# Performance work log

Hardware: AMD Instinct MI355X
Metric: run time of the kernel (lower is better)

## Reference

```python
import jax, jax.numpy as jnp
import numpy as np


def setup_inputs() -> dict:
    key = jax.random.key(0)
    ks = jax.random.split(key, 6)
    B, Cin, H, W = 8, 512, 128, 128
    Ck, Cv, K = 256, 256, 64
    s = lambda fan: fan ** -0.5
    return {
        "x": jax.random.normal(ks[0], (B, Cin, H, W), jnp.float32),
        "context": jax.random.normal(ks[1], (B, Cv, K), jnp.float32),
        "Wq": jax.random.normal(ks[2], (Ck, Cin), jnp.float32) * s(Cin),
        "Wk": jax.random.normal(ks[3], (Ck, Cv), jnp.float32) * s(Cv),
        "Wv": jax.random.normal(ks[4], (Cv, Cv), jnp.float32) * s(Cv),
        "Wp": jax.random.normal(ks[5], (Cin, Cv), jnp.float32) * s(Cv),
    }


def reference(x, context, Wq, Wk, Wv, Wp):
    B, Cin, H, W = x.shape
    Ck = Wq.shape[0]
    scale = Ck ** -0.5
    xf = x.reshape(B, Cin, H * W)                      # [B, Cin, N]
    q = jnp.einsum("kc,bcn->bnk", Wq, xf)             # [B, N, Ck]
    k = jnp.einsum("kc,bcm->bkm", Wk, context)        # [B, Ck, K]
    v = jnp.einsum("vc,bcm->bmv", Wv, context)        # [B, K, Cv]
    sim = jnp.einsum("bnk,bkm->bnm", q, k) * scale    # [B, N, K]
    attn = jax.nn.softmax(sim, axis=-1)
    out = jnp.einsum("bnm,bmv->bnv", attn, v)         # [B, N, Cv]
    out = jnp.einsum("cv,bnv->bcn", Wp, out)          # [B, Cin, N]
    return out.reshape(B, Cin, H, W)
```

## Files before the change

### kernel.cpp

```cpp
#include <hip/hip_runtime.h>
#include <stdint.h>

#define B_    8
#define CIN   512
#define NPIX  16384
#define CK    256
#define KCTX  64
#define CV    256

typedef _Float16 f16;
typedef _Float16 f16x4 __attribute__((ext_vector_type(4)));
typedef _Float16 f16x8 __attribute__((ext_vector_type(8)));
typedef float    f32x4 __attribute__((ext_vector_type(4)));

#define LOG2E 1.44269504f

#define WQK_OFF 0
#define WPV_OFF 524288

#define WAITVM(N) asm volatile("s_waitcnt vmcnt(" #N ")" ::: "memory")
#define LGKM0     asm volatile("s_waitcnt lgkmcnt(0)" ::: "memory")
#define SCHEDB    __builtin_amdgcn_sched_barrier(0)
#define SBAR      __builtin_amdgcn_s_barrier()

__device__ __forceinline__ void gl_lds16(const void* g, void* l) {
    __builtin_amdgcn_global_load_lds(
        (const __attribute__((address_space(1))) uint32_t*)g,
        (__attribute__((address_space(3))) uint32_t*)l, 16, 0, 0);
}

__global__ __launch_bounds__(1024) void prep(const float* __restrict__ ctx,
                                             const float* __restrict__ Wk,
                                             const float* __restrict__ Wv,
                                             const float* __restrict__ Wq,
                                             const float* __restrict__ Wp,
                                             char* __restrict__ ws) {
    __shared__ char lds[65536];
    char* ctx_t = lds;
    char* kv_s  = lds + 32768;

    const int p = blockIdx.x;
    const int b = blockIdx.y;
    const int path = p >> 1, h = p & 1;
    const int t = threadIdx.x;
    const int w = t >> 6, l = t & 63, g = l >> 4, ln = l & 15;

    {
        const int m4 = (t & 15) * 4, c4 = (t >> 4) * 4;
        const float* cp = ctx + (size_t)b * (CV * KCTX) + (size_t)c4 * KCTX + m4;
        f32x4 xr[4];
        #pragma unroll
        for (int i = 0; i < 4; ++i) xr[i] = *(const f32x4*)(cp + (size_t)i * KCTX);
        #pragma unroll
        for (int j = 0; j < 4; ++j) {
            f16x4 v4; v4[0] = (f16)xr[0][j]; v4[1] = (f16)xr[1][j]; v4[2] = (f16)xr[2][j]; v4[3] = (f16)xr[3][j];
            int m = m4 + j;
            *(f16x4*)(ctx_t + m * 512 + 16 * (((c4 >> 3) & 31) ^ (m & 7)) + 2 * (c4 & 7)) = v4;
        }
    }
    __syncthreads();

    {
        const float* W = path ? Wv : Wk;
        const int rbase = 64 * (w >> 2);
        const int mm = 16 * (w & 3) + ln;
        f32x4 acc[4] = {};
        for (int ks = 0; ks < 8; ++ks) {
            f16x8 bf = *(const f16x8*)(ctx_t + mm * 512 + 16 * ((4 * ks + g) ^ (mm & 7)));
            #pragma unroll
            for (int mi = 0; mi < 4; ++mi) {
                int row = rbase + 16 * mi + ln;
                const float* wp0 = W + (size_t)row * CV + 32 * ks + 8 * g;
                f32x4 lo = *(const f32x4*)wp0, hi = *(const f32x4*)(wp0 + 4);
                f16x8 af;
                #pragma unroll
                for (int j = 0; j < 4; ++j) { af[j] = (f16)lo[j]; af[4 + j] = (f16)hi[j]; }
                acc[mi] = __builtin_amdgcn_mfma_f32_16x16x32_f16(af, bf, acc[mi], 0, 0, 0);
            }
        }
        #pragma unroll
        for (int mi = 0; mi < 4; ++mi)
            #pragma unroll
            for (int r = 0; r < 4; ++r) {
                int row = rbase + 16 * mi + 4 * g + r;
                *(f16*)(kv_s + mm * 512 + 16 * ((((row >> 3) & 31)) ^ (mm & 7)) + 2 * (row & 7)) = (f16)acc[mi][r];
            }
    }
    __syncthreads();

    if (path == 0) {
        f32x4 acc2[4] = {};
        const int cA = 256 * h + 16 * w + ln;
        const float* qcol = Wq + cA;
        for (int ks = 0; ks < 8; ++ks) {
            f16x8 af;
            #pragma unroll
            for (int j = 0; j < 8; ++j)
                af[j] = (f16)qcol[(size_t)(32 * ks + 8 * g + j) * CIN];
            #pragma unroll
            for (int ni = 0; ni < 4; ++ni) {
                int m2 = 16 * ni + ln;
                f16x8 bf = *(const f16x8*)(kv_s + m2 * 512 + 16 * ((4 * ks + g) ^ (m2 & 7)));
                acc2[ni] = __builtin_amdgcn_mfma_f32_16x16x32_f16(af, bf, acc2[ni], 0, 0, 0);
            }
        }
        char* dst = ws + WQK_OFF + b * 65536;
        #pragma unroll
        for (int ni = 0; ni < 4; ++ni)
            #pragma unroll
            for (int r = 0; r < 4; ++r) {
                int c = 256 * h + 16 * w + 4 * g + r;
                int s  = c >> 6, kk = (c >> 5) & 1, gk = (c >> 3) & 3, j = c & 7;
                int byte = ((((s * 4 + ni) * 2 + kk) * 4 + gk) * 16 + ln) * 16 + 2 * j;
                *(f16*)(dst + byte) = (f16)(acc2[ni][r] * 0.0625f);
            }
    } else {
        f32x4 acc2[4] = {};
        const int cA = 256 * h + 16 * w + ln;
        for (int ks = 0; ks < 8; ++ks) {
            const float* pp = Wp + (size_t)cA * CV + 32 * ks + 8 * g;
            f32x4 lo = *(const f32x4*)pp, hi = *(const f32x4*)(pp + 4);
            f16x8 af;
            #pragma unroll
            for (int j = 0; j < 4; ++j) { af[j] = (f16)lo[j]; af[4 + j] = (f16)hi[j]; }
            #pragma unroll
            for (int ni = 0; ni < 4; ++ni) {
                int m2 = 16 * ni + ln;
                f16x8 bf = *(const f16x8*)(kv_s + m2 * 512 + 16 * ((4 * ks + g) ^ (m2 & 7)));
                acc2[ni] = __builtin_amdgcn_mfma_f32_16x16x32_f16(af, bf, acc2[ni], 0, 0, 0);
            }
        }
        char* dst = ws + WPV_OFF + b * 65536;
        #pragma unroll
        for (int ni = 0; ni < 4; ++ni) {
            const int kkm = ni >> 1;
            const int gm  = ln >> 2;
            const int jm  = 4 * (ni & 1) + (ln & 3);
            #pragma unroll
            for (int r = 0; r < 4; ++r) {
                int c = 256 * h + 16 * w + 4 * g + r;
                int ct = c >> 4, lnc = c & 15;
                int byte = (((ct * 2 + kkm) * 4 + gm) * 16 + lnc) * 16 + 2 * jm;
                *(f16*)(dst + byte) = (f16)acc2[ni][r];
            }
        }
    }
}

__global__ __launch_bounds__(1024) void fused(const float* __restrict__ x,
                                              const char* __restrict__ ws,
                                              float* __restrict__ out) {
    extern __shared__ char lds[];
    char* tab_l = lds;
    char* x_s   = lds + 65536;

    const int b = blockIdx.y;
    const int n0 = blockIdx.x * 256;
    const int t = threadIdx.x;
    const int w = t >> 6, l = t & 63, g = l >> 4, ln = l & 15;
    const int nB = 16 * w + ln;
    const int fnB = (nB ^ (nB >> 3)) & 7;

    const char* wqk_g = ws + WQK_OFF + b * 65536;
    const char* wpv_g = ws + WPV_OFF + b * 65536;
    const float* xb = x + (size_t)b * CIN * NPIX + n0;

    const int cg = t >> 6;
    const int n4 = 4 * (t & 63);

    f32x4 xr[2][4];

#define STAGE_LOAD(S, SLOT)                                                    \
    {                                                                          \
        const float* xp = xb + (size_t)(64 * (S) + 4 * cg) * NPIX + n4;        \
        asm volatile("global_load_dwordx4 %0, %1, off"                        \
                     : "=&v"(xr[SLOT][0]) : "v"(xp));                          \
        asm volatile("global_load_dwordx4 %0, %1, off"                        \
                     : "=&v"(xr[SLOT][1]) : "v"(xp + NPIX));                   \
        asm volatile("global_load_dwordx4 %0, %1, off"                        \
                     : "=&v"(xr[SLOT][2]) : "v"(xp + 2 * (size_t)NPIX));       \
        asm volatile("global_load_dwordx4 %0, %1, off"                        \
                     : "=&v"(xr[SLOT][3]) : "v"(xp + 3 * (size_t)NPIX));       \
    }

#define STAGE_WRITE(BUF, SLOT)                                                 \
    {                                                                          \
        _Pragma("unroll")                                                      \
        for (int j = 0; j < 4; ++j) {                                          \
            f16x4 v4;                                                          \
            v4[0] = (f16)xr[SLOT][0][j]; v4[1] = (f16)xr[SLOT][1][j];          \
            v4[2] = (f16)xr[SLOT][2][j]; v4[3] = (f16)xr[SLOT][3][j];          \
            int nl = n4 + j;                                                   \
            int fn = (nl ^ (nl >> 3)) & 7;                                     \
            *(f16x4*)((BUF) + nl * 128 + 16 * ((cg >> 1) ^ fn) + 8 * (cg & 1)) = v4; \
        }                                                                      \
    }

    #pragma unroll
    for (int r = 0; r < 4; ++r) {
        int ch = t + 1024 * r;
        gl_lds16(wqk_g + ch * 16, tab_l + ch * 16);
    }
    SCHEDB;
    STAGE_LOAD(0, 0); SCHEDB;
    STAGE_LOAD(1, 1); SCHEDB;
    WAITVM(4);
    SCHEDB;
    STAGE_WRITE(x_s, 0);
    LGKM0; SCHEDB; SBAR; SCHEDB;

    f32x4 accs[4] = {};
    #pragma unroll
    for (int s = 0; s < 8; ++s) {
        const char* xc = x_s + (s & 1) * 32768;
        #pragma unroll
        for (int kk = 0; kk < 2; ++kk) {
            f16x8 bf = *(const f16x8*)(xc + nB * 128 + 16 * ((4 * kk + g) ^ fnB));
            #pragma unroll
            for (int mi = 0; mi < 4; ++mi) {
                f16x8 af = *(const f16x8*)(tab_l + ((((s * 4 + mi) * 2 + kk) * 4 + g) * 16 + ln) * 16);
                accs[mi] = __builtin_amdgcn_mfma_f32_16x16x32_f16(af, bf, accs[mi], 0, 0, 0);
            }
        }
        SCHEDB;
        if (s < 7) {
            if (s < 6) { STAGE_LOAD(s + 2, (s & 1)); SCHEDB; }
            if (s < 6) { WAITVM(4); } else { WAITVM(0); }
            SCHEDB;
            STAGE_WRITE(x_s + ((s + 1) & 1) * 32768, ((s + 1) & 1));
            LGKM0;
        } else {
            LGKM0;
        }
        SCHEDB; SBAR; SCHEDB;
    }

    #pragma unroll
    for (int r = 0; r < 4; ++r) {
        int ch = t + 1024 * r;
        gl_lds16(wpv_g + ch * 16, tab_l + ch * 16);
    }

    float mx = accs[0][0];
    #pragma unroll
    for (int mi = 0; mi < 4; ++mi)
        #pragma unroll
        for (int r = 0; r < 4; ++r) mx = fmaxf(mx, accs[mi][r]);
    mx = fmaxf(mx, __shfl_xor(mx, 16, 64));
    mx = fmaxf(mx, __shfl_xor(mx, 32, 64));
    float pv[4][4];
    float sum = 0.f;
    #pragma unroll
    for (int mi = 0; mi < 4; ++mi)
        #pragma unroll
        for (int r = 0; r < 4; ++r) {
            float pe = __builtin_amdgcn_exp2f((accs[mi][r] - mx) * LOG2E);
            pv[mi][r] = pe; sum += pe;
        }
    sum += __shfl_xor(sum, 16, 64);
    sum += __shfl_xor(sum, 32, 64);
    float inv = 1.f / sum;

    f16x8 afr[2];
    #pragma unroll
    for (int kk = 0; kk < 2; ++kk)
        #pragma unroll
        for (int j = 0; j < 8; ++j)
            afr[kk][j] = (f16)(pv[2 * kk + (j >> 2)][j & 3] * inv);

    WAITVM(0); SCHEDB; SBAR; SCHEDB;

    float* ob = out + (size_t)b * CIN * NPIX + n0 + 16 * w + 4 * g;
    #pragma unroll 4
    for (int ct = 0; ct < 32; ++ct) {
        int c = 16 * ct + ln;
        f32x4 acc = {};
        #pragma unroll
        for (int kk = 0; kk < 2; ++kk) {
            f16x8 bfp = *(const f16x8*)(tab_l + (((ct * 2 + kk) * 4 + g) * 16 + ln) * 16);
            acc = __builtin_amdgcn_mfma_f32_16x16x32_f16(afr[kk], bfp, acc, 0, 0, 0);
        }
        *(f32x4*)(ob + (size_t)c * NPIX) = acc;
    }
}

extern "C" void kernel_launch(void* const* d_in, const int* in_sizes, int n_in,
                              void* d_out, int out_size, void* d_ws, size_t ws_size,
                              hipStream_t stream) {
    (void)in_sizes; (void)n_in; (void)out_size; (void)ws_size;
    const float* x   = (const float*)d_in[0];
    const float* ctx = (const float*)d_in[1];
    const float* Wq  = (const float*)d_in[2];
    const float* Wk  = (const float*)d_in[3];
    const float* Wv  = (const float*)d_in[4];
    const float* Wp  = (const float*)d_in[5];
    float* out = (float*)d_out;
    char* ws = (char*)d_ws;

    prep<<<dim3(4, B_), 1024, 0, stream>>>(ctx, Wk, Wv, Wq, Wp, ws);
    fused<<<dim3(NPIX / 256, B_), 1024, 131072, stream>>>(x, ws, out);
}
```

Baseline: 161.6 us.

## Double pixel tile per block and reuse weight fragments across two n-tiles

```diff
diff --git a/kernel.cpp b/kernel.cpp
--- a/kernel.cpp
+++ b/kernel.cpp
@@ -15,8 +15,8 @@
 
 #define LOG2E 1.44269504f
 
-#define WQK_OFF 0
-#define WPV_OFF 524288
+#define WQK_OFF  0
+#define WPV_OFF  524288
 
 #define WAITVM(N) asm volatile("s_waitcnt vmcnt(" #N ")" ::: "memory")
 #define LGKM0     asm volatile("s_waitcnt lgkmcnt(0)" ::: "memory")
@@ -151,28 +151,30 @@
                                               const char* __restrict__ ws,
                                               float* __restrict__ out) {
     extern __shared__ char lds[];
-    char* tab_l = lds;
+    char* wqk_l = lds;
     char* x_s   = lds + 65536;
-
-    const int b = blockIdx.y;
-    const int n0 = blockIdx.x * 256;
-    const int t = threadIdx.x;
-    const int w = t >> 6, l = t & 63, g = l >> 4, ln = l & 15;
-    const int nB = 16 * w + ln;
-    const int fnB = (nB ^ (nB >> 3)) & 7;
+    char* wpv_l = lds + 65536;
+
+    const int b  = blockIdx.y;
+    const int n0 = blockIdx.x * 512;
+    const int t  = threadIdx.x;
+    const int w  = t >> 6, l = t & 63, g = l >> 4, ln = l & 15;
 
     const char* wqk_g = ws + WQK_OFF + b * 65536;
     const char* wpv_g = ws + WPV_OFF + b * 65536;
     const float* xb = x + (size_t)b * CIN * NPIX + n0;
 
-    const int cg = t >> 6;
-    const int n4 = 4 * (t & 63);
+    const int n4 = 4 * (t & 127);
+    const int u  = t >> 7;
+    const int rowbase = 4 * u;
+    const int wslot_hi = u >> 1;
+    const int wslot_lo = 8 * (u & 1);
 
     f32x4 xr[2][4];
 
 #define STAGE_LOAD(S, SLOT)                                                    \
     {                                                                          \
-        const float* xp = xb + (size_t)(64 * (S) + 4 * cg) * NPIX + n4;        \
+        const float* xp = xb + (size_t)(32 * (S) + rowbase) * NPIX + n4;       \
         asm volatile("global_load_dwordx4 %0, %1, off"                        \
                      : "=&v"(xr[SLOT][0]) : "v"(xp));                          \
         asm volatile("global_load_dwordx4 %0, %1, off"                        \
@@ -191,15 +193,15 @@
             v4[0] = (f16)xr[SLOT][0][j]; v4[1] = (f16)xr[SLOT][1][j];          \
             v4[2] = (f16)xr[SLOT][2][j]; v4[3] = (f16)xr[SLOT][3][j];          \
             int nl = n4 + j;                                                   \
-            int fn = (nl ^ (nl >> 3)) & 7;                                     \
-            *(f16x4*)((BUF) + nl * 128 + 16 * ((cg >> 1) ^ fn) + 8 * (cg & 1)) = v4; \
+            int fn2 = (nl ^ (nl >> 2)) & 3;                                    \
+            *(f16x4*)((BUF) + nl * 64 + 16 * ((wslot_hi ^ fn2) & 3) + wslot_lo) = v4; \
         }                                                                      \
     }
 
     #pragma unroll
     for (int r = 0; r < 4; ++r) {
         int ch = t + 1024 * r;
-        gl_lds16(wqk_g + ch * 16, tab_l + ch * 16);
+        gl_lds16(wqk_g + ch * 16, wqk_l + ch * 16);
     }
     SCHEDB;
     STAGE_LOAD(0, 0); SCHEDB;
@@ -209,78 +211,84 @@
     STAGE_WRITE(x_s, 0);
     LGKM0; SCHEDB; SBAR; SCHEDB;
 
-    f32x4 accs[4] = {};
+    f32x4 accs[2][4] = {};
     #pragma unroll
-    for (int s = 0; s < 8; ++s) {
-        const char* xc = x_s + (s & 1) * 32768;
-        #pragma unroll
-        for (int kk = 0; kk < 2; ++kk) {
-            f16x8 bf = *(const f16x8*)(xc + nB * 128 + 16 * ((4 * kk + g) ^ fnB));
-            #pragma unroll
-            for (int mi = 0; mi < 4; ++mi) {
-                f16x8 af = *(const f16x8*)(tab_l + ((((s * 4 + mi) * 2 + kk) * 4 + g) * 16 + ln) * 16);
-                accs[mi] = __builtin_amdgcn_mfma_f32_16x16x32_f16(af, bf, accs[mi], 0, 0, 0);
-            }
+    for (int cc = 0; cc < 16; ++cc) {
+        const char* xc = x_s + (cc & 1) * 32768;
+        f16x8 bf[2];
+        #pragma unroll
+        for (int nt = 0; nt < 2; ++nt) {
+            int nl = 32 * w + 16 * nt + ln;
+            int fn2 = (nl ^ (nl >> 2)) & 3;
+            bf[nt] = *(const f16x8*)(xc + nl * 64 + 16 * ((g ^ fn2) & 3));
+        }
+        #pragma unroll
+        for (int mi = 0; mi < 4; ++mi) {
+            f16x8 af = *(const f16x8*)(wqk_l +
+                ((((cc >> 1) * 4 + mi) * 2 + (cc & 1)) * 4 + g) * 256 + ln * 16);
+            accs[0][mi] = __builtin_amdgcn_mfma_f32_16x16x32_f16(af, bf[0], accs[0][mi], 0, 0, 0);
+            accs[1][mi] = __builtin_amdgcn_mfma_f32_16x16x32_f16(af, bf[1], accs[1][mi], 0, 0, 0);
         }
         SCHEDB;
-        if (s < 7) {
-            if (s < 6) { STAGE_LOAD(s + 2, (s & 1)); SCHEDB; }
-            if (s < 6) { WAITVM(4); } else { WAITVM(0); }
+        if (cc < 14) { STAGE_LOAD(cc + 2, cc & 1); SCHEDB; }
+        if (cc < 15) {
+            if (cc < 14) { WAITVM(4); } else { WAITVM(0); }
             SCHEDB;
-            STAGE_WRITE(x_s + ((s + 1) & 1) * 32768, ((s + 1) & 1));
-            LGKM0;
-        } else {
-            LGKM0;
-        }
-        SCHEDB; SBAR; SCHEDB;
-    }
+            STAGE_WRITE(x_s + ((cc + 1) & 1) * 32768, (cc + 1) & 1);
+            LGKM0; SCHEDB; SBAR; SCHEDB;
+        }
+    }
+    LGKM0; SCHEDB; SBAR; SCHEDB;
 
     #pragma unroll
     for (int r = 0; r < 4; ++r) {
         int ch = t + 1024 * r;
-        gl_lds16(wpv_g + ch * 16, tab_l + ch * 16);
-    }
-
-    float mx = accs[0][0];
+        gl_lds16(wpv_g + ch * 16, wpv_l + ch * 16);
+    }
+
+    f16x8 afr[2][2];
     #pragma unroll
-    for (int mi = 0; mi < 4; ++mi)
-        #pragma unroll
-        for (int r = 0; r < 4; ++r) mx = fmaxf(mx, accs[mi][r]);
-    mx = fmaxf(mx, __shfl_xor(mx, 16, 64));
-    mx = fmaxf(mx, __shfl_xor(mx, 32, 64));
-    float pv[4][4];
-    float sum = 0.f;
-    #pragma unroll
-    for (int mi = 0; mi < 4; ++mi)
-        #pragma unroll
-        for (int r = 0; r < 4; ++r) {
-            float pe = __builtin_amdgcn_exp2f((accs[mi][r] - mx) * LOG2E);
-            pv[mi][r] = pe; sum += pe;
-        }
-    sum += __shfl_xor(sum, 16, 64);
-    sum += __shfl_xor(sum, 32, 64);
-    float inv = 1.f / sum;
-
-    f16x8 afr[2];
-    #pragma unroll
-    for (int kk = 0; kk < 2; ++kk)
-        #pragma unroll
-        for (int j = 0; j < 8; ++j)
-            afr[kk][j] = (f16)(pv[2 * kk + (j >> 2)][j & 3] * inv);
-
+    for (int nt = 0; nt < 2; ++nt) {
+        float mx = accs[nt][0][0];
+        #pragma unroll
+        for (int mi = 0; mi < 4; ++mi)
+            #pragma unroll
+            for (int r = 0; r < 4; ++r) mx = fmaxf(mx, accs[nt][mi][r]);
+        mx = fmaxf(mx, __shfl_xor(mx, 16, 64));
+        mx = fmaxf(mx, __shfl_xor(mx, 32, 64));
+        float pv[4][4];
+        float sum = 0.f;
+        #pragma unroll
+        for (int mi = 0; mi < 4; ++mi)
+            #pragma unroll
+            for (int r = 0; r < 4; ++r) {
+                float pe = __builtin_amdgcn_exp2f((accs[nt][mi][r] - mx) * LOG2E);
+                pv[mi][r] = pe; sum += pe;
+            }
+        sum += __shfl_xor(sum, 16, 64);
+        sum += __shfl_xor(sum, 32, 64);
+        float inv = 1.f / sum;
+        #pragma unroll
+        for (int kk = 0; kk < 2; ++kk)
+            #pragma unroll
+            for (int j = 0; j < 8; ++j)
+                afr[nt][kk][j] = (f16)(pv[2 * kk + (j >> 2)][j & 3] * inv);
+    }
     WAITVM(0); SCHEDB; SBAR; SCHEDB;
 
-    float* ob = out + (size_t)b * CIN * NPIX + n0 + 16 * w + 4 * g;
+    float* ob = out + (size_t)b * CIN * NPIX + n0 + 32 * w + 4 * g;
     #pragma unroll 4
     for (int ct = 0; ct < 32; ++ct) {
         int c = 16 * ct + ln;
-        f32x4 acc = {};
+        f32x4 a0 = {}, a1 = {};
         #pragma unroll
         for (int kk = 0; kk < 2; ++kk) {
-            f16x8 bfp = *(const f16x8*)(tab_l + (((ct * 2 + kk) * 4 + g) * 16 + ln) * 16);
-            acc = __builtin_amdgcn_mfma_f32_16x16x32_f16(afr[kk], bfp, acc, 0, 0, 0);
-        }
-        *(f32x4*)(ob + (size_t)c * NPIX) = acc;
+            f16x8 bfp = *(const f16x8*)(wpv_l + (((ct * 2 + kk) * 4 + g) * 16 + ln) * 16);
+            a0 = __builtin_amdgcn_mfma_f32_16x16x32_f16(afr[0][kk], bfp, a0, 0, 0, 0);
+            a1 = __builtin_amdgcn_mfma_f32_16x16x32_f16(afr[1][kk], bfp, a1, 0, 0, 0);
+        }
+        *(f32x4*)(ob + (size_t)c * NPIX)      = a0;
+        *(f32x4*)(ob + (size_t)c * NPIX + 16) = a1;
     }
 }
 
@@ -298,5 +306,5 @@
     char* ws = (char*)d_ws;
 
     prep<<<dim3(4, B_), 1024, 0, stream>>>(ctx, Wk, Wv, Wq, Wp, ws);
-    fused<<<dim3(NPIX / 256, B_), 1024, 131072, stream>>>(x, ws, out);
+    fused<<<dim3(NPIX / 512, B_), 1024, 131072, stream>>>(x, ws, out);
 }
```

After: 180.8 us. 1.12x slower.
